# Kernel optimization log

Measured on AMD Instinct MI355X. Metric: run time of the kernel, lower is better.

Reference implementation:

```python
import jax, jax.numpy as jnp
import numpy as np

MASK_OD = np.array([
    [False, False, False, True, True, True, True, False, False],
    [False, False, True, True, True, True, True, True, False],
    [False, True, True, True, True, True, True, True, True],
    [True, True, True, True, True, True, True, False, True],
    [True, True, True, True, True, True, True, False, True],
    [False, True, True, True, True, True, True, True, True],
    [False, False, True, True, True, True, True, True, False],
    [False, False, False, True, True, True, True, False, False]], dtype=bool)

SCALE = float(np.sqrt(128.0))  # sqrt(attn_dim)


def build_prior(num_points=52):
    # Faithful reproduction of _init_anatomical_prior (OD laterality, no flip)
    pr_grid = np.arange(196) // 14
    pc_grid = np.arange(196) % 14
    prior = np.zeros((num_points, 196), dtype=np.float32)
    vf_idx = 0
    for r in range(8):
        for c in range(9):
            if MASK_OD[r, c]:
                pr = 13 - int(r * 13 / 7)
                pc = 13 - int(c * 13 / 8)
                prior[vf_idx] = -((pr_grid - pr) ** 2 + (pc_grid - pc) ** 2) / (2.0 * 3.0 ** 2)
                vf_idx += 1
    return prior


def setup_inputs() -> dict:
    key = jax.random.key(0)
    ks = jax.random.split(key, 8)
    B, P, K, E, A = 256, 52, 196, 1024, 128
    return {
        "patches": jax.random.normal(ks[0], (B, K, E), jnp.float32),
        "queries": jax.random.normal(ks[1], (P, A), jnp.float32) * 0.02,
        "Wk": jax.random.normal(ks[2], (A, E), jnp.float32) / np.sqrt(E),
        "Wv": jax.random.normal(ks[3], (A, E), jnp.float32) / np.sqrt(E),
        "Wo": jax.random.normal(ks[4], (E, A), jnp.float32) / np.sqrt(A),
        "bo": jnp.zeros((E,), jnp.float32),
        "patch_pos": jax.random.normal(ks[5], (K, A), jnp.float32) * 0.02,
        "temperature": jnp.asarray(2.0, jnp.float32),
        "attn_prior": jnp.asarray(build_prior(P)),
    }


def reference(patches, queries, Wk, Wv, Wo, bo, patch_pos, temperature, attn_prior):
    # patches: [B, 196, E]; laterality fixed to 'OD' (no prior flip)
    keys = jnp.einsum('bke,ae->bka', patches, Wk) + patch_pos  # [B, 196, A]
    vals = jnp.einsum('bke,ae->bka', patches, Wv)              # [B, 196, A]
    logits = jnp.einsum('qa,bka->bqk', queries, keys) / SCALE  # [B, 52, 196]
    temp = jax.nn.softplus(temperature) + 0.5
    logits = (logits + attn_prior[None]) / temp
    attn_weights = jax.nn.softmax(logits, axis=-1)
    # dropout is identity in eval mode
    attended = jnp.einsum('bqk,bka->bqa', attn_weights, vals)  # [B, 52, A]
    out = jnp.einsum('bqa,ea->bqe', attended, Wo) + bo         # [B, 52, E]
    return out, attn_weights
```

## Files before the change

### kernel.cpp

```cpp
#include <hip/hip_runtime.h>

typedef __attribute__((ext_vector_type(8))) short bf16x8;
typedef __attribute__((ext_vector_type(4))) short bf16x4;
typedef __attribute__((ext_vector_type(4))) float f32x4;
typedef __attribute__((ext_vector_type(4))) float floatx4;

__device__ __forceinline__ unsigned short f2bf(float f) {
    unsigned int u = __float_as_uint(f);
    u += 0x7fffu + ((u >> 16) & 1u);
    return (unsigned short)(u >> 16);
}
__device__ __forceinline__ float bf2f_s(short h) {
    return __uint_as_float(((unsigned int)(unsigned short)h) << 16);
}

__global__ void k_convert(const float* __restrict__ Wk, const float* __restrict__ Wv,
                          const float* __restrict__ Wo,
                          unsigned short* __restrict__ Wkvb, unsigned short* __restrict__ Wob) {
    int i = blockIdx.x * blockDim.x + threadIdx.x;
    if (i < 131072) {
        Wkvb[i]          = f2bf(Wk[i]);
        Wkvb[131072 + i] = f2bf(Wv[i]);
        Wob[i]           = f2bf(Wo[i]);
    }
}

__global__ __launch_bounds__(512)
void k_keysvals(const float* __restrict__ patches,
                const unsigned short* __restrict__ Wkvb,
                const float* __restrict__ patch_pos,
                unsigned short* __restrict__ kv)
{
    __shared__ unsigned short As[64][72];
    __shared__ unsigned short Bs[256][72];

    const int tid  = threadIdx.x;
    const int lane = tid & 63;
    const int wave = tid >> 6;
    const int wm   = wave >> 2;
    const int wn   = wave & 3;
    const int l15  = lane & 15;
    const int lg   = lane >> 4;
    const int row0 = blockIdx.x * 64;

    f32x4 acc[2][4];
    #pragma unroll
    for (int i = 0; i < 2; ++i)
        #pragma unroll
        for (int j = 0; j < 4; ++j)
            acc[i][j] = (f32x4){0.f, 0.f, 0.f, 0.f};

    for (int ko = 0; ko < 1024; ko += 64) {
        {
            int r = tid >> 4;
            int c = (tid & 15) * 4;
            #pragma unroll
            for (int it = 0; it < 2; ++it) {
                floatx4 v = *reinterpret_cast<const floatx4*>(
                    patches + (size_t)(row0 + it * 32 + r) * 1024 + ko + c);
                bf16x4 sv;
                sv[0] = (short)f2bf(v[0]); sv[1] = (short)f2bf(v[1]);
                sv[2] = (short)f2bf(v[2]); sv[3] = (short)f2bf(v[3]);
                *reinterpret_cast<bf16x4*>(&As[it * 32 + r][c]) = sv;
            }
        }
        {
            int r = tid >> 3;
            int c = (tid & 7) * 8;
            #pragma unroll
            for (int it = 0; it < 4; ++it) {
                bf16x8 v = *reinterpret_cast<const bf16x8*>(
                    Wkvb + (size_t)(it * 64 + r) * 1024 + ko + c);
                *reinterpret_cast<bf16x8*>(&Bs[it * 64 + r][c]) = v;
            }
        }
        __syncthreads();
        #pragma unroll
        for (int kk = 0; kk < 2; ++kk) {
            bf16x8 af[2], bfr[4];
            #pragma unroll
            for (int mi = 0; mi < 2; ++mi)
                af[mi] = *reinterpret_cast<const bf16x8*>(&As[wm * 32 + mi * 16 + l15][kk * 32 + lg * 8]);
            #pragma unroll
            for (int ni = 0; ni < 4; ++ni)
                bfr[ni] = *reinterpret_cast<const bf16x8*>(&Bs[wn * 64 + ni * 16 + l15][kk * 32 + lg * 8]);
            #pragma unroll
            for (int mi = 0; mi < 2; ++mi)
                #pragma unroll
                for (int ni = 0; ni < 4; ++ni)
                    acc[mi][ni] = __builtin_amdgcn_mfma_f32_16x16x32_bf16(af[mi], bfr[ni], acc[mi][ni], 0, 0, 0);
        }
        __syncthreads();
    }
    #pragma unroll
    for (int mi = 0; mi < 2; ++mi) {
        #pragma unroll
        for (int i = 0; i < 4; ++i) {
            int m  = row0 + wm * 32 + mi * 16 + lg * 4 + i;
            int kp = m % 196;
            #pragma unroll
            for (int ni = 0; ni < 4; ++ni) {
                int n = wn * 64 + ni * 16 + l15;
                float v = acc[mi][ni][i];
                if (n < 128) v += patch_pos[kp * 128 + n];
                kv[(size_t)m * 256 + n] = f2bf(v);
            }
        }
    }
}

__global__ __launch_bounds__(1024)
void k_attn(const unsigned short* __restrict__ kv,
            const float* __restrict__ queries,
            const float* __restrict__ prior,
            const float* __restrict__ temperature,
            float* __restrict__ attn_out,
            unsigned short* __restrict__ att)
{
    __shared__ unsigned short k_s[196][136];
    __shared__ unsigned short v_s[196][128];
    __shared__ unsigned short q_s[52][128];
    __shared__ float          l_s[52][196];

    const int b   = blockIdx.x;
    const int tid = threadIdx.x;
    const size_t base = (size_t)b * 196 * 256;

    for (int idx = tid; idx < 6272; idx += 1024) {
        int row = idx >> 5;
        int c   = (idx & 31) * 8;
        bf16x8 v = *reinterpret_cast<const bf16x8*>(kv + base + row * 256 + c);
        if (c < 128) *reinterpret_cast<bf16x8*>(&k_s[row][c])       = v;
        else         *reinterpret_cast<bf16x8*>(&v_s[row][c - 128]) = v;
    }
    for (int idx = tid; idx < 1664; idx += 1024) {
        int row = idx >> 5;
        int c   = (idx & 31) * 4;
        const float* qp = queries + row * 128 + c;
        bf16x4 sv;
        sv[0] = (short)f2bf(qp[0]); sv[1] = (short)f2bf(qp[1]);
        sv[2] = (short)f2bf(qp[2]); sv[3] = (short)f2bf(qp[3]);
        *reinterpret_cast<bf16x4*>(&q_s[row][c]) = sv;
    }
    __syncthreads();

    const float inv_temp  = 1.0f / (log1pf(expf(temperature[0])) + 0.5f);
    const float inv_scale = 0.08838834764831845f;

    for (int task = tid; task < 3328; task += 1024) {
        int q  = task >> 6;
        int kg = task & 63;
        if (kg < 49) {
            float dot0 = 0.f, dot1 = 0.f, dot2 = 0.f, dot3 = 0.f;
            #pragma unroll 4
            for (int c = 0; c < 128; c += 8) {
                bf16x8 qv = *reinterpret_cast<const bf16x8*>(&q_s[q][c]);
                float qf[8];
                #pragma unroll
                for (int e = 0; e < 8; ++e) qf[e] = bf2f_s(qv[e]);
                bf16x8 k0v = *reinterpret_cast<const bf16x8*>(&k_s[kg][c]);
                bf16x8 k1v = *reinterpret_cast<const bf16x8*>(&k_s[kg + 49][c]);
                bf16x8 k2v = *reinterpret_cast<const bf16x8*>(&k_s[kg + 98][c]);
                bf16x8 k3v = *reinterpret_cast<const bf16x8*>(&k_s[kg + 147][c]);
                #pragma unroll
                for (int e = 0; e < 8; ++e) {
                    dot0 += qf[e] * bf2f_s(k0v[e]);
                    dot1 += qf[e] * bf2f_s(k1v[e]);
                    dot2 += qf[e] * bf2f_s(k2v[e]);
                    dot3 += qf[e] * bf2f_s(k3v[e]);
                }
            }
            int k;
            k = kg;       l_s[q][k] = (dot0 * inv_scale + prior[q * 196 + k]) * inv_temp;
            k = kg + 49;  l_s[q][k] = (dot1 * inv_scale + prior[q * 196 + k]) * inv_temp;
            k = kg + 98;  l_s[q][k] = (dot2 * inv_scale + prior[q * 196 + k]) * inv_temp;
            k = kg + 147; l_s[q][k] = (dot3 * inv_scale + prior[q * 196 + k]) * inv_temp;
        }
    }
    __syncthreads();

    const int lane = tid & 63;
    const int wave = tid >> 6;
    for (int q = wave; q < 52; q += 16) {
        float x0 = l_s[q][lane];
        float x1 = l_s[q][lane + 64];
        float x2 = l_s[q][lane + 128];
        float x3 = (lane < 4) ? l_s[q][lane + 192] : -1e30f;
        float m = fmaxf(fmaxf(x0, x1), fmaxf(x2, x3));
        #pragma unroll
        for (int off = 32; off > 0; off >>= 1) m = fmaxf(m, __shfl_xor(m, off));
        float e0 = expf(x0 - m), e1 = expf(x1 - m), e2 = expf(x2 - m);
        float e3 = (lane < 4) ? expf(x3 - m) : 0.0f;
        float s = e0 + e1 + e2 + e3;
        #pragma unroll
        for (int off = 32; off > 0; off >>= 1) s += __shfl_xor(s, off);
        float inv = 1.0f / s;
        float* po = attn_out + ((size_t)b * 52 + q) * 196;
        float a0 = e0 * inv, a1 = e1 * inv, a2 = e2 * inv;
        l_s[q][lane]       = a0;  po[lane]       = a0;
        l_s[q][lane + 64]  = a1;  po[lane + 64]  = a1;
        l_s[q][lane + 128] = a2;  po[lane + 128] = a2;
        if (lane < 4) { float a3 = e3 * inv; l_s[q][lane + 192] = a3; po[lane + 192] = a3; }
    }
    __syncthreads();

    if (tid < 832) {
        int q  = tid >> 4;
        int a0 = (tid & 15) * 8;
        float accv[8] = {0.f, 0.f, 0.f, 0.f, 0.f, 0.f, 0.f, 0.f};
        for (int k = 0; k < 196; ++k) {
            float w = l_s[q][k];
            bf16x8 vv = *reinterpret_cast<const bf16x8*>(&v_s[k][a0]);
            #pragma unroll
            for (int e = 0; e < 8; ++e) accv[e] += w * bf2f_s(vv[e]);
        }
        bf16x8 sv;
        #pragma unroll
        for (int e = 0; e < 8; ++e) sv[e] = (short)f2bf(accv[e]);
        *reinterpret_cast<bf16x8*>(att + ((size_t)b * 52 + q) * 128 + a0) = sv;
    }
}

__global__ __launch_bounds__(512)
void k_out(const unsigned short* __restrict__ att,
           const unsigned short* __restrict__ Wob,
           const float* __restrict__ bo,
           float* __restrict__ out)
{
    __shared__ unsigned short As[64][72];
    __shared__ unsigned short Bs[256][72];

    const int tid  = threadIdx.x;
    const int lane = tid & 63;
    const int wave = tid >> 6;
    const int wm   = wave >> 2;
    const int wn   = wave & 3;
    const int l15  = lane & 15;
    const int lg   = lane >> 4;
    const int row0 = blockIdx.x * 64;
    const int e0   = blockIdx.y * 256;

    f32x4 acc[2][4];
    #pragma unroll
    for (int i = 0; i < 2; ++i)
        #pragma unroll
        for (int j = 0; j < 4; ++j)
            acc[i][j] = (f32x4){0.f, 0.f, 0.f, 0.f};

    for (int ko = 0; ko < 128; ko += 64) {
        {
            int r = tid >> 3;
            int c = (tid & 7) * 8;
            bf16x8 v = *reinterpret_cast<const bf16x8*>(att + (size_t)(row0 + r) * 128 + ko + c);
            *reinterpret_cast<bf16x8*>(&As[r][c]) = v;
        }
        {
            int r = tid >> 3;
            int c = (tid & 7) * 8;
            #pragma unroll
            for (int it = 0; it < 4; ++it) {
                bf16x8 v = *reinterpret_cast<const bf16x8*>(Wob + (size_t)(e0 + it * 64 + r) * 128 + ko + c);
                *reinterpret_cast<bf16x8*>(&Bs[it * 64 + r][c]) = v;
            }
        }
        __syncthreads();
        #pragma unroll
        for (int kk = 0; kk < 2; ++kk) {
            bf16x8 af[2], bfr[4];
            #pragma unroll
            for (int mi = 0; mi < 2; ++mi)
                af[mi] = *reinterpret_cast<const bf16x8*>(&As[wm * 32 + mi * 16 + l15][kk * 32 + lg * 8]);
            #pragma unroll
            for (int ni = 0; ni < 4; ++ni)
                bfr[ni] = *reinterpret_cast<const bf16x8*>(&Bs[wn * 64 + ni * 16 + l15][kk * 32 + lg * 8]);
            #pragma unroll
            for (int mi = 0; mi < 2; ++mi)
                #pragma unroll
                for (int ni = 0; ni < 4; ++ni)
                    acc[mi][ni] = __builtin_amdgcn_mfma_f32_16x16x32_bf16(af[mi], bfr[ni], acc[mi][ni], 0, 0, 0);
        }
        __syncthreads();
    }
    #pragma unroll
    for (int mi = 0; mi < 2; ++mi) {
        #pragma unroll
        for (int i = 0; i < 4; ++i) {
            int m = row0 + wm * 32 + mi * 16 + lg * 4 + i;
            #pragma unroll
            for (int ni = 0; ni < 4; ++ni) {
                int e = e0 + wn * 64 + ni * 16 + l15;
                out[(size_t)m * 1024 + e] = acc[mi][ni][i] + bo[e];
            }
        }
    }
}

extern "C" void kernel_launch(void* const* d_in, const int* in_sizes, int n_in,
                              void* d_out, int out_size, void* d_ws, size_t ws_size,
                              hipStream_t stream)
{
    const float* patches     = (const float*)d_in[0];
    const float* queries     = (const float*)d_in[1];
    const float* Wk          = (const float*)d_in[2];
    const float* Wv          = (const float*)d_in[3];
    const float* Wo          = (const float*)d_in[4];
    const float* bo          = (const float*)d_in[5];
    const float* patch_pos   = (const float*)d_in[6];
    const float* temperature = (const float*)d_in[7];
    const float* prior       = (const float*)d_in[8];

    float* out      = (float*)d_out;
    float* attn_out = out + (size_t)256 * 52 * 1024;

    unsigned short* Wkvb = (unsigned short*)d_ws;
    unsigned short* Wob  = Wkvb + 256 * 1024;
    unsigned short* kv   = Wob + 1024 * 128;
    unsigned short* att  = kv + (size_t)50176 * 256;

    k_convert <<<512, 256, 0, stream>>>(Wk, Wv, Wo, Wkvb, Wob);
    k_keysvals<<<784, 512, 0, stream>>>(patches, Wkvb, patch_pos, kv);
    k_attn    <<<256, 1024, 0, stream>>>(kv, queries, prior, temperature, attn_out, att);
    k_out     <<<dim3(208, 4), 512, 0, stream>>>(att, Wob, bo, out);
}
```

Before: 161.6 us.

## Double-buffer keys/values GEMM with register B, LDS-free output GEMM, vectorized convert

The keys/values GEMM now keeps weight fragments in registers, loaded straight from global memory, and double-buffers only the converted patch tile in LDS. Next-tile loads are prefetched before the MFMAs, which halves the barriers per iteration. The output projection drops LDS staging and has each wave load its own fragments from global memory over a smaller 32x64 tile, and the weight conversion kernel is vectorized four-wide. The costs are more global-load traffic for the weights, since waves sharing columns reload them, and higher register pressure under the new occupancy hint.

```diff
diff --git a/kernel.cpp b/kernel.cpp
--- a/kernel.cpp
+++ b/kernel.cpp
@@ -17,22 +17,29 @@
 __global__ void k_convert(const float* __restrict__ Wk, const float* __restrict__ Wv,
                           const float* __restrict__ Wo,
                           unsigned short* __restrict__ Wkvb, unsigned short* __restrict__ Wob) {
-    int i = blockIdx.x * blockDim.x + threadIdx.x;
+    int i = (blockIdx.x * blockDim.x + threadIdx.x) * 4;
     if (i < 131072) {
-        Wkvb[i]          = f2bf(Wk[i]);
-        Wkvb[131072 + i] = f2bf(Wv[i]);
-        Wob[i]           = f2bf(Wo[i]);
-    }
-}
-
-__global__ __launch_bounds__(512)
+        floatx4 a = *reinterpret_cast<const floatx4*>(Wk + i);
+        floatx4 b = *reinterpret_cast<const floatx4*>(Wv + i);
+        floatx4 c = *reinterpret_cast<const floatx4*>(Wo + i);
+        bf16x4 sa, sb, sc;
+        #pragma unroll
+        for (int e = 0; e < 4; ++e) {
+            sa[e] = (short)f2bf(a[e]); sb[e] = (short)f2bf(b[e]); sc[e] = (short)f2bf(c[e]);
+        }
+        *reinterpret_cast<bf16x4*>(Wkvb + i)          = sa;
+        *reinterpret_cast<bf16x4*>(Wkvb + 131072 + i) = sb;
+        *reinterpret_cast<bf16x4*>(Wob + i)           = sc;
+    }
+}
+
+__global__ __launch_bounds__(512, 4)
 void k_keysvals(const float* __restrict__ patches,
                 const unsigned short* __restrict__ Wkvb,
                 const float* __restrict__ patch_pos,
                 unsigned short* __restrict__ kv)
 {
-    __shared__ unsigned short As[64][72];
-    __shared__ unsigned short Bs[256][72];
+    __shared__ unsigned short As[2][64][80];
 
     const int tid  = threadIdx.x;
     const int lane = tid & 63;
@@ -43,6 +50,12 @@
     const int lg   = lane >> 4;
     const int row0 = blockIdx.x * 64;
 
+    const int ar = tid >> 3;
+    const int ac = (tid & 7) * 8;
+    const float* aptr = patches + (size_t)(row0 + ar) * 1024 + ac;
+
+    const unsigned short* bptr = Wkvb + (size_t)(wn * 64 + l15) * 1024 + lg * 8;
+
     f32x4 acc[2][4];
     #pragma unroll
     for (int i = 0; i < 2; ++i)
@@ -50,48 +63,61 @@
         for (int j = 0; j < 4; ++j)
             acc[i][j] = (f32x4){0.f, 0.f, 0.f, 0.f};
 
-    for (int ko = 0; ko < 1024; ko += 64) {
-        {
-            int r = tid >> 4;
-            int c = (tid & 15) * 4;
-            #pragma unroll
-            for (int it = 0; it < 2; ++it) {
-                floatx4 v = *reinterpret_cast<const floatx4*>(
-                    patches + (size_t)(row0 + it * 32 + r) * 1024 + ko + c);
-                bf16x4 sv;
-                sv[0] = (short)f2bf(v[0]); sv[1] = (short)f2bf(v[1]);
-                sv[2] = (short)f2bf(v[2]); sv[3] = (short)f2bf(v[3]);
-                *reinterpret_cast<bf16x4*>(&As[it * 32 + r][c]) = sv;
-            }
-        }
-        {
-            int r = tid >> 3;
-            int c = (tid & 7) * 8;
-            #pragma unroll
-            for (int it = 0; it < 4; ++it) {
-                bf16x8 v = *reinterpret_cast<const bf16x8*>(
-                    Wkvb + (size_t)(it * 64 + r) * 1024 + ko + c);
-                *reinterpret_cast<bf16x8*>(&Bs[it * 64 + r][c]) = v;
-            }
-        }
-        __syncthreads();
+    floatx4 a0, a1;
+    bf16x8 breg[2][4];
+
+    a0 = *reinterpret_cast<const floatx4*>(aptr);
+    a1 = *reinterpret_cast<const floatx4*>(aptr + 4);
+    #pragma unroll
+    for (int kk = 0; kk < 2; ++kk)
+        #pragma unroll
+        for (int ni = 0; ni < 4; ++ni)
+            breg[kk][ni] = *reinterpret_cast<const bf16x8*>(bptr + (size_t)ni * 16 * 1024 + kk * 32);
+    {
+        bf16x8 sv;
+        #pragma unroll
+        for (int e = 0; e < 4; ++e) { sv[e] = (short)f2bf(a0[e]); sv[4 + e] = (short)f2bf(a1[e]); }
+        *reinterpret_cast<bf16x8*>(&As[0][ar][ac]) = sv;
+    }
+    __syncthreads();
+
+    int cur = 0;
+    for (int t = 0; t < 16; ++t) {
+        const int konext = (t + 1) * 64;
+        if (t < 15) {
+            a0 = *reinterpret_cast<const floatx4*>(aptr + konext);
+            a1 = *reinterpret_cast<const floatx4*>(aptr + konext + 4);
+        }
+        __builtin_amdgcn_sched_barrier(0);
+
         #pragma unroll
         for (int kk = 0; kk < 2; ++kk) {
-            bf16x8 af[2], bfr[4];
+            bf16x8 af[2];
             #pragma unroll
             for (int mi = 0; mi < 2; ++mi)
-                af[mi] = *reinterpret_cast<const bf16x8*>(&As[wm * 32 + mi * 16 + l15][kk * 32 + lg * 8]);
-            #pragma unroll
-            for (int ni = 0; ni < 4; ++ni)
-                bfr[ni] = *reinterpret_cast<const bf16x8*>(&Bs[wn * 64 + ni * 16 + l15][kk * 32 + lg * 8]);
+                af[mi] = *reinterpret_cast<const bf16x8*>(&As[cur][wm * 32 + mi * 16 + l15][kk * 32 + lg * 8]);
             #pragma unroll
             for (int mi = 0; mi < 2; ++mi)
                 #pragma unroll
                 for (int ni = 0; ni < 4; ++ni)
-                    acc[mi][ni] = __builtin_amdgcn_mfma_f32_16x16x32_bf16(af[mi], bfr[ni], acc[mi][ni], 0, 0, 0);
-        }
-        __syncthreads();
-    }
+                    acc[mi][ni] = __builtin_amdgcn_mfma_f32_16x16x32_bf16(af[mi], breg[kk][ni], acc[mi][ni], 0, 0, 0);
+        }
+
+        if (t < 15) {
+            #pragma unroll
+            for (int kk = 0; kk < 2; ++kk)
+                #pragma unroll
+                for (int ni = 0; ni < 4; ++ni)
+                    breg[kk][ni] = *reinterpret_cast<const bf16x8*>(bptr + (size_t)ni * 16 * 1024 + konext + kk * 32);
+            bf16x8 sv;
+            #pragma unroll
+            for (int e = 0; e < 4; ++e) { sv[e] = (short)f2bf(a0[e]); sv[4 + e] = (short)f2bf(a1[e]); }
+            *reinterpret_cast<bf16x8*>(&As[cur ^ 1][ar][ac]) = sv;
+            __syncthreads();
+            cur ^= 1;
+        }
+    }
+
     #pragma unroll
     for (int mi = 0; mi < 2; ++mi) {
         #pragma unroll
@@ -221,24 +247,20 @@
     }
 }
 
-__global__ __launch_bounds__(512)
+__global__ __launch_bounds__(256)
 void k_out(const unsigned short* __restrict__ att,
            const unsigned short* __restrict__ Wob,
            const float* __restrict__ bo,
            float* __restrict__ out)
 {
-    __shared__ unsigned short As[64][72];
-    __shared__ unsigned short Bs[256][72];
-
-    const int tid  = threadIdx.x;
-    const int lane = tid & 63;
-    const int wave = tid >> 6;
-    const int wm   = wave >> 2;
-    const int wn   = wave & 3;
+    const int w    = (blockIdx.x * 256 + threadIdx.x) >> 6;
+    const int lane = threadIdx.x & 63;
     const int l15  = lane & 15;
     const int lg   = lane >> 4;
-    const int row0 = blockIdx.x * 64;
-    const int e0   = blockIdx.y * 256;
+    const int mt   = w % 416;
+    const int et   = w / 416;
+    const int m0   = mt * 32;
+    const int e0   = et * 64;
 
     f32x4 acc[2][4];
     #pragma unroll
@@ -247,50 +269,36 @@
         for (int j = 0; j < 4; ++j)
             acc[i][j] = (f32x4){0.f, 0.f, 0.f, 0.f};
 
-    for (int ko = 0; ko < 128; ko += 64) {
-        {
-            int r = tid >> 3;
-            int c = (tid & 7) * 8;
-            bf16x8 v = *reinterpret_cast<const bf16x8*>(att + (size_t)(row0 + r) * 128 + ko + c);
-            *reinterpret_cast<bf16x8*>(&As[r][c]) = v;
-        }
-        {
-            int r = tid >> 3;
-            int c = (tid & 7) * 8;
-            #pragma unroll
-            for (int it = 0; it < 4; ++it) {
-                bf16x8 v = *reinterpret_cast<const bf16x8*>(Wob + (size_t)(e0 + it * 64 + r) * 128 + ko + c);
-                *reinterpret_cast<bf16x8*>(&Bs[it * 64 + r][c]) = v;
-            }
-        }
-        __syncthreads();
-        #pragma unroll
-        for (int kk = 0; kk < 2; ++kk) {
-            bf16x8 af[2], bfr[4];
-            #pragma unroll
-            for (int mi = 0; mi < 2; ++mi)
-                af[mi] = *reinterpret_cast<const bf16x8*>(&As[wm * 32 + mi * 16 + l15][kk * 32 + lg * 8]);
+    const unsigned short* ap = att + (size_t)(m0 + l15) * 128 + lg * 8;
+    const unsigned short* bp = Wob + (size_t)(e0 + l15) * 128 + lg * 8;
+
+    #pragma unroll
+    for (int kk = 0; kk < 4; ++kk) {
+        bf16x8 af[2], bfr[4];
+        af[0] = *reinterpret_cast<const bf16x8*>(ap + kk * 32);
+        af[1] = *reinterpret_cast<const bf16x8*>(ap + 16 * 128 + kk * 32);
+        #pragma unroll
+        for (int ni = 0; ni < 4; ++ni)
+            bfr[ni] = *reinterpret_cast<const bf16x8*>(bp + (size_t)ni * 16 * 128 + kk * 32);
+        #pragma unroll
+        for (int mi = 0; mi < 2; ++mi)
             #pragma unroll
             for (int ni = 0; ni < 4; ++ni)
-                bfr[ni] = *reinterpret_cast<const bf16x8*>(&Bs[wn * 64 + ni * 16 + l15][kk * 32 + lg * 8]);
-            #pragma unroll
-            for (int mi = 0; mi < 2; ++mi)
-                #pragma unroll
-                for (int ni = 0; ni < 4; ++ni)
-                    acc[mi][ni] = __builtin_amdgcn_mfma_f32_16x16x32_bf16(af[mi], bfr[ni], acc[mi][ni], 0, 0, 0);
-        }
-        __syncthreads();
-    }
+                acc[mi][ni] = __builtin_amdgcn_mfma_f32_16x16x32_bf16(af[mi], bfr[ni], acc[mi][ni], 0, 0, 0);
+    }
+
+    float bov[4];
+    #pragma unroll
+    for (int ni = 0; ni < 4; ++ni) bov[ni] = bo[e0 + ni * 16 + l15];
+
     #pragma unroll
     for (int mi = 0; mi < 2; ++mi) {
         #pragma unroll
         for (int i = 0; i < 4; ++i) {
-            int m = row0 + wm * 32 + mi * 16 + lg * 4 + i;
-            #pragma unroll
-            for (int ni = 0; ni < 4; ++ni) {
-                int e = e0 + wn * 64 + ni * 16 + l15;
-                out[(size_t)m * 1024 + e] = acc[mi][ni][i] + bo[e];
-            }
+            int m = m0 + mi * 16 + lg * 4 + i;
+            #pragma unroll
+            for (int ni = 0; ni < 4; ++ni)
+                out[(size_t)m * 1024 + e0 + ni * 16 + l15] = acc[mi][ni][i] + bov[ni];
         }
     }
 }
@@ -317,8 +325,8 @@
     unsigned short* kv   = Wob + 1024 * 128;
     unsigned short* att  = kv + (size_t)50176 * 256;
 
-    k_convert <<<512, 256, 0, stream>>>(Wk, Wv, Wo, Wkvb, Wob);
+    k_convert <<<128, 256, 0, stream>>>(Wk, Wv, Wo, Wkvb, Wob);
     k_keysvals<<<784, 512, 0, stream>>>(patches, Wkvb, patch_pos, kv);
     k_attn    <<<256, 1024, 0, stream>>>(kv, queries, prior, temperature, attn_out, att);
-    k_out     <<<dim3(208, 4), 512, 0, stream>>>(att, Wob, bo, out);
-}
+    k_out     <<<dim3(1664), 256, 0, stream>>>(att, Wob, bo, out);
+}
```

Result: slower. 232.8 us (+44.0%).
